# Performance work log

Hardware: AMD Instinct MI355X
Metric: run time of the kernel (lower is better)

The kernel has to match this reference:

```python
import jax, jax.numpy as jnp
import numpy as np

B, N, K, U = 64, 4096, 32, 16
NUM_STEPS = 8
NUM_CLASSES = 2


def setup_inputs() -> dict:
    key = jax.random.key(0)
    ks = jax.random.split(key, 17)
    s = 0.05
    g = lambda k, shape: jax.random.normal(k, shape, dtype=jnp.float32) * s
    return {
        "inputs": jax.random.normal(ks[0], (B, N, K + 2), dtype=jnp.float32),
        # UGRNN cell params
        "Wn": g(ks[1], (K, U)),
        "Wg": g(ks[2], (U, U)), "Ug": g(ks[3], (U, U)), "bg": jnp.zeros((U,), jnp.float32),
        "Wc": g(ks[4], (U, U)), "Uc": g(ks[5], (U, U)), "bc": jnp.zeros((U,), jnp.float32),
        "We": g(ks[6], (U, U)), "be": jnp.zeros((U,), jnp.float32),
        # MLP head (Dropout is identity at inference)
        "W1": g(ks[7], (N * U, 256)), "b1": jnp.zeros((256,), jnp.float32),
        "W2": g(ks[8], (256, 32)),    "b2": jnp.zeros((32,), jnp.float32),
        "W3": g(ks[9], (32, NUM_CLASSES)), "b3": jnp.zeros((NUM_CLASSES,), jnp.float32),
    }


def reference(inputs, Wn, Wg, Ug, bg, Wc, Uc, bc, We, be, W1, b1, W2, b2, W3, b3):
    # split channels: node scalar, K neighbour features, edge scalar
    h0 = inputs[..., 0]            # [B, N]
    neigh = inputs[..., 1:-1]      # [B, N, K]
    e0 = inputs[..., -1]           # [B, N]

    units = Wg.shape[0]
    h = jnp.broadcast_to(h0[..., None], h0.shape + (units,))  # tile -> [B, N, U]
    e = jnp.broadcast_to(e0[..., None], e0.shape + (units,))  # tile -> [B, N, U]

    # neighbour aggregation/projection is constant across steps -> hoist
    m = jnp.einsum("bnk,ku->bnu", neigh, Wn)  # [B, N, U]

    for _ in range(NUM_STEPS):  # small fixed unroll over num_steps
        x = m + e
        g = jax.nn.sigmoid(x @ Wg + h @ Ug + bg)  # update gate
        c = jnp.tanh(x @ Wc + h @ Uc + bc)        # candidate
        h = g * h + (1.0 - g) * c                 # UGRNN update
        e = jnp.tanh(x @ We + be)                 # edge state update

    out = h.reshape(h.shape[0], -1)               # Flatten -> [B, N*U]
    out = jax.nn.relu(out @ W1 + b1)
    out = jax.nn.relu(out @ W2 + b2)
    return jax.nn.softmax(out @ W3 + b3, axis=-1)  # [B, num_classes]
```

## Files before the change

kernel.cpp:

```cpp
#include <hip/hip_runtime.h>

typedef _Float16 half8_t __attribute__((ext_vector_type(8)));
typedef _Float16 half4_t __attribute__((ext_vector_type(4)));
typedef __fp16   fp16x2  __attribute__((ext_vector_type(2)));
typedef float    f32x4  __attribute__((ext_vector_type(4)));

#define MFMA32(a, b, c) __builtin_amdgcn_mfma_f32_16x16x32_f16((a), (b), (c), 0, 0, 0)
#define MFMA16(a, b, c) __builtin_amdgcn_mfma_f32_16x16x16f16((a), (b), (c), 0, 0, 0)

__device__ __forceinline__ void load_lds16(const void* g, void* l) {
    __builtin_amdgcn_global_load_lds(
        (const __attribute__((address_space(1))) unsigned int*)g,
        (__attribute__((address_space(3))) unsigned int*)l, 16, 0, 0);
}
__device__ __forceinline__ void load_lds4(const void* g, void* l) {
    __builtin_amdgcn_global_load_lds(
        (const __attribute__((address_space(1))) unsigned int*)g,
        (__attribute__((address_space(3))) unsigned int*)l, 4, 0, 0);
}

__device__ __forceinline__ half4_t pk4(f32x4 v) {
    fp16x2 lo = __builtin_amdgcn_cvt_pkrtz(v[0], v[1]);
    fp16x2 hi = __builtin_amdgcn_cvt_pkrtz(v[2], v[3]);
    half4_t r;
    r[0] = (_Float16)lo[0]; r[1] = (_Float16)lo[1];
    r[2] = (_Float16)hi[0]; r[3] = (_Float16)hi[1];
    return r;
}

__device__ __forceinline__ f32x4 exp2v(f32x4 v) {
    f32x4 r;
    r[0] = __builtin_amdgcn_exp2f(v[0]);
    r[1] = __builtin_amdgcn_exp2f(v[1]);
    r[2] = __builtin_amdgcn_exp2f(v[2]);
    r[3] = __builtin_amdgcn_exp2f(v[3]);
    return r;
}
__device__ __forceinline__ f32x4 rcpv(f32x4 v) {
    f32x4 r;
    r[0] = __builtin_amdgcn_rcpf(v[0]);
    r[1] = __builtin_amdgcn_rcpf(v[1]);
    r[2] = __builtin_amdgcn_rcpf(v[2]);
    r[3] = __builtin_amdgcn_rcpf(v[3]);
    return r;
}

__global__
__attribute__((amdgpu_flat_work_group_size(256, 256)))
void ugrnn_mfma(
    const float* __restrict__ inputs,
    const float* __restrict__ Wn, const float* __restrict__ Wg,
    const float* __restrict__ Ug, const float* __restrict__ bg,
    const float* __restrict__ Wc, const float* __restrict__ Uc,
    const float* __restrict__ bc, const float* __restrict__ We,
    const float* __restrict__ be, _Float16* __restrict__ h_t)
{
    __shared__ float raw[4][1088];

    const int wave = threadIdx.x >> 6;
    const int lane = threadIdx.x & 63;
    const int t16  = lane & 15;
    const int q    = lane >> 4;

    const int pair = blockIdx.x * 4 + wave;
    const int b    = pair >> 7;
    const int n0   = (pair & 127) << 5;

    const float* gsrc = inputs + (size_t)pair * 1088;
    float* buf = raw[wave];
#pragma unroll
    for (int k2 = 0; k2 < 4; ++k2)
        load_lds16(gsrc + k2 * 256 + lane * 4, buf + k2 * 256);
    load_lds4(gsrc + 1024 + lane, buf + 1024);

    const float NL2E = -1.44269504f;
    const float TL2E =  2.88539008f;

    half8_t An;
#pragma unroll
    for (int i = 0; i < 8; ++i)
        An[i] = (_Float16)Wn[(q * 8 + i) * 16 + t16];

    half4_t Awg, Aug, Awc, Auc, Awe;
#pragma unroll
    for (int i = 0; i < 4; ++i) {
        const int k = 4 * q + i;
        Awg[i] = (_Float16)(Wg[k * 16 + t16] * NL2E);
        Aug[i] = (_Float16)(Ug[k * 16 + t16] * NL2E);
        Awc[i] = (_Float16)(Wc[k * 16 + t16] * TL2E);
        Auc[i] = (_Float16)(Uc[k * 16 + t16] * TL2E);
        Awe[i] = (_Float16)(We[k * 16 + t16] * TL2E);
    }
    f32x4 bgC, bcC, beC;
#pragma unroll
    for (int r = 0; r < 4; ++r) {
        bgC[r] = bg[4 * q + r] * NL2E;
        bcC[r] = bc[4 * q + r] * TL2E;
        beC[r] = be[4 * q + r] * TL2E;
    }

    asm volatile("s_waitcnt vmcnt(0)" ::: "memory");
    __builtin_amdgcn_sched_barrier(0);

    f32x4 m[2], h[2], e[2];
    const f32x4 zc = {0.f, 0.f, 0.f, 0.f};
#pragma unroll
    for (int u2 = 0; u2 < 2; ++u2) {
        const float* rp = buf + u2 * 544;
        half8_t Bx;
#pragma unroll
        for (int i = 0; i < 8; ++i)
            Bx[i] = (_Float16)rp[t16 * 34 + 1 + q * 8 + i];
        m[u2] = MFMA32(An, Bx, zc);
        const float hv = rp[t16 * 34 + 0];
        const float ev = rp[t16 * 34 + 33];
        h[u2] = (f32x4){hv, hv, hv, hv};
        e[u2] = (f32x4){ev, ev, ev, ev};
    }

    const f32x4 one = {1.f, 1.f, 1.f, 1.f};

#pragma unroll 1
    for (int step = 0; step < 8; ++step) {
        f32x4 gp[2], cp[2], ep[2];
#pragma unroll
        for (int u2 = 0; u2 < 2; ++u2) {
            const f32x4 x = m[u2] + e[u2];
            half4_t xB = pk4(x);
            half4_t hB = pk4(h[u2]);
            f32x4 g1 = MFMA16(Awg, xB, bgC);
            f32x4 g2 = MFMA16(Aug, hB, zc);
            f32x4 c1 = MFMA16(Awc, xB, bcC);
            f32x4 c2 = MFMA16(Auc, hB, zc);
            gp[u2] = g1 + g2;
            cp[u2] = c1 + c2;
            if (step < 7) ep[u2] = MFMA16(Awe, xB, beC);
        }
#pragma unroll
        for (int u2 = 0; u2 < 2; ++u2) {
            const f32x4 Ae = one + exp2v(gp[u2]);
            const f32x4 Be = one + exp2v(cp[u2]);
            if (step < 7) {
                const f32x4 Ce = one + exp2v(ep[u2]);
                const f32x4 BC = Be * Ce;
                const f32x4 rr = rcpv(Ae * BC);
                const f32x4 gv = rr * BC;
                const f32x4 cv = one - 2.0f * (rr * (Ae * Ce));
                h[u2] = cv + gv * (h[u2] - cv);
                e[u2] = one - 2.0f * (rr * (Ae * Be));
            } else {
                const f32x4 rr = rcpv(Ae * Be);
                const f32x4 gv = rr * Be;
                const f32x4 cv = one - 2.0f * (rr * Ae);
                h[u2] = cv + gv * (h[u2] - cv);
            }
        }
    }

#pragma unroll
    for (int u2 = 0; u2 < 2; ++u2)
        *(half4_t*)(h_t + (size_t)b * 65536
                        + (size_t)(n0 + u2 * 16 + t16) * 16 + 4 * q) =
            pk4(h[u2]);
}

__global__
__attribute__((amdgpu_flat_work_group_size(256, 256)))
void fc1_mfma(const _Float16* __restrict__ h_t, const float* __restrict__ W1,
              _Float16* __restrict__ partials)
{
    __shared__ float w1s[2][32][258];
    const int tid  = threadIdx.x;
    const int wave = tid >> 6;
    const int lane = tid & 63;
    const int t16  = lane & 15;
    const int q    = lane >> 4;
    const int i0   = blockIdx.x * 128;

    f32x4 acc[4][4];
#pragma unroll
    for (int mt = 0; mt < 4; ++mt)
#pragma unroll
        for (int nt = 0; nt < 4; ++nt)
            acc[mt][nt] = (f32x4){0.f, 0.f, 0.f, 0.f};

#pragma unroll
    for (int r = 0; r < 8; ++r) {
        int row = wave * 8 + r;
        load_lds16(W1 + (size_t)(i0 + row) * 256 + lane * 4, &w1s[0][row][0]);
    }
    __syncthreads();

#pragma unroll 1
    for (int c = 0; c < 4; ++c) {
        const int buf = c & 1;
        const int cb  = i0 + c * 32;

        half8_t A[4];
#pragma unroll
        for (int mt = 0; mt < 4; ++mt)
            A[mt] = *(const half8_t*)(h_t
                + (size_t)(mt * 16 + t16) * 65536 + cb + q * 8);

        if (c < 3) {
#pragma unroll
            for (int r = 0; r < 8; ++r) {
                int row = wave * 8 + r;
                load_lds16(W1 + (size_t)(cb + 32 + row) * 256 + lane * 4,
                           &w1s[buf ^ 1][row][0]);
            }
        }

#pragma unroll
        for (int nt = 0; nt < 4; ++nt) {
            int j = (wave * 4 + nt) * 16 + t16;
            half8_t Bf;
#pragma unroll
            for (int i = 0; i < 8; ++i)
                Bf[i] = (_Float16)w1s[buf][q * 8 + i][j];
#pragma unroll
            for (int mt = 0; mt < 4; ++mt)
                acc[mt][nt] = MFMA32(A[mt], Bf, acc[mt][nt]);
        }
        __syncthreads();
    }

    _Float16* pb = partials + (size_t)blockIdx.x * 16384;
#pragma unroll
    for (int mt = 0; mt < 4; ++mt)
#pragma unroll
        for (int nt = 0; nt < 4; ++nt)
#pragma unroll
            for (int r = 0; r < 4; ++r)
                pb[(mt * 16 + 4 * q + r) * 256 + (wave * 4 + nt) * 16 + t16] =
                    (_Float16)acc[mt][nt][r];
}

__global__ __launch_bounds__(1024) void mlp_tail(
    const _Float16* __restrict__ partials, const float* __restrict__ b1,
    const float* __restrict__ W2, const float* __restrict__ b2,
    const float* __restrict__ W3, const float* __restrict__ b3,
    float* __restrict__ out)
{
    __shared__ float x1p[16][256];
    __shared__ float x1s[256];
    __shared__ float x2q[32][33];
    __shared__ float x2s[32];
    __shared__ float lg[2];
    const int b = blockIdx.x, tid = threadIdx.x;
    const int kg = tid >> 6, l64 = tid & 63;
    const int j0 = l64 * 4;

    const _Float16* p = partials + (size_t)(kg * 32) * 16384 + (size_t)b * 256 + j0;
    float s0 = 0.f, s1 = 0.f, s2 = 0.f, s3 = 0.f;
#pragma unroll
    for (int k = 0; k < 32; ++k) {
        half4_t v = *(const half4_t*)(p + (size_t)k * 16384);
        s0 += (float)v[0]; s1 += (float)v[1]; s2 += (float)v[2]; s3 += (float)v[3];
    }
    x1p[kg][j0 + 0] = s0;
    x1p[kg][j0 + 1] = s1;
    x1p[kg][j0 + 2] = s2;
    x1p[kg][j0 + 3] = s3;
    __syncthreads();

    if (tid < 256) {
        float t = b1[tid];
#pragma unroll
        for (int g = 0; g < 16; ++g) t += x1p[g][tid];
        x1s[tid] = fmaxf(t, 0.f);
    }
    __syncthreads();

    const int j2 = tid & 31, g2 = tid >> 5;
    float s = 0.f;
#pragma unroll
    for (int k = g2 * 8; k < g2 * 8 + 8; ++k) s += x1s[k] * W2[k * 32 + j2];
    x2q[g2][j2] = s;
    __syncthreads();
    if (tid < 32) {
        float t = b2[tid];
#pragma unroll
        for (int g = 0; g < 32; ++g) t += x2q[g][tid];
        x2s[tid] = fmaxf(t, 0.f);
    }
    __syncthreads();
    if (tid < 2) {
        float t = b3[tid];
#pragma unroll
        for (int k = 0; k < 32; ++k) t += x2s[k] * W3[k * 2 + tid];
        lg[tid] = t;
    }
    __syncthreads();
    if (tid == 0) {
        float mx = fmaxf(lg[0], lg[1]);
        float e0 = __expf(lg[0] - mx), e1 = __expf(lg[1] - mx);
        float inv = 1.0f / (e0 + e1);
        out[b * 2 + 0] = e0 * inv;
        out[b * 2 + 1] = e1 * inv;
    }
}

extern "C" void kernel_launch(void* const* d_in, const int* in_sizes, int n_in,
                              void* d_out, int out_size, void* d_ws, size_t ws_size,
                              hipStream_t stream) {
    const float* inputs = (const float*)d_in[0];
    const float* Wn = (const float*)d_in[1];
    const float* Wg = (const float*)d_in[2];
    const float* Ug = (const float*)d_in[3];
    const float* bg = (const float*)d_in[4];
    const float* Wc = (const float*)d_in[5];
    const float* Uc = (const float*)d_in[6];
    const float* bc = (const float*)d_in[7];
    const float* We = (const float*)d_in[8];
    const float* be = (const float*)d_in[9];
    const float* W1 = (const float*)d_in[10];
    const float* b1 = (const float*)d_in[11];
    const float* W2 = (const float*)d_in[12];
    const float* b2 = (const float*)d_in[13];
    const float* W3 = (const float*)d_in[14];
    const float* b3 = (const float*)d_in[15];
    float* out = (float*)d_out;

    _Float16* h_t      = (_Float16*)d_ws;
    _Float16* partials = (_Float16*)((char*)d_ws + (size_t)64 * 65536 * 2);

    ugrnn_mfma<<<2048, 256, 0, stream>>>(inputs, Wn, Wg, Ug, bg, Wc, Uc, bc,
                                         We, be, h_t);
    fc1_mfma<<<512, 256, 0, stream>>>(h_t, W1, partials);
    mlp_tail<<<64, 1024, 0, stream>>>(partials, b1, W2, b2, W3, b3, out);
}
```

Measured before the change: 185.2 us.

## Fuse UGRNN recurrence with FC1 partial GEMM in one kernel

Merges the recurrence kernel and the first dense layer into one kernel. Each block now handles 4 nodes across all 64 batches, keeps h in LDS, and multiplies it directly against the matching 64 rows of W1, so the h_t round trip through global memory and one launch go away. The cost is a partials buffer 1024-deep instead of 512-deep, which makes the tail reduction read twice as many partials. W1 is now read straight from global memory with strided scalar loads instead of being staged through LDS, and the block grows to 512 threads with a waves-per-EU hint.

After: 246.9 us. 1.33x slower.

```diff
diff --git a/kernel.cpp b/kernel.cpp
--- a/kernel.cpp
+++ b/kernel.cpp
@@ -7,17 +7,6 @@
 
 #define MFMA32(a, b, c) __builtin_amdgcn_mfma_f32_16x16x32_f16((a), (b), (c), 0, 0, 0)
 #define MFMA16(a, b, c) __builtin_amdgcn_mfma_f32_16x16x16f16((a), (b), (c), 0, 0, 0)
-
-__device__ __forceinline__ void load_lds16(const void* g, void* l) {
-    __builtin_amdgcn_global_load_lds(
-        (const __attribute__((address_space(1))) unsigned int*)g,
-        (__attribute__((address_space(3))) unsigned int*)l, 16, 0, 0);
-}
-__device__ __forceinline__ void load_lds4(const void* g, void* l) {
-    __builtin_amdgcn_global_load_lds(
-        (const __attribute__((address_space(1))) unsigned int*)g,
-        (__attribute__((address_space(3))) unsigned int*)l, 4, 0, 0);
-}
 
 __device__ __forceinline__ half4_t pk4(f32x4 v) {
     fp16x2 lo = __builtin_amdgcn_cvt_pkrtz(v[0], v[1]);
@@ -27,7 +16,6 @@
     r[2] = (_Float16)hi[0]; r[3] = (_Float16)hi[1];
     return r;
 }
-
 __device__ __forceinline__ f32x4 exp2v(f32x4 v) {
     f32x4 r;
     r[0] = __builtin_amdgcn_exp2f(v[0]);
@@ -46,32 +34,47 @@
 }
 
 __global__
-__attribute__((amdgpu_flat_work_group_size(256, 256)))
-void ugrnn_mfma(
+__attribute__((amdgpu_flat_work_group_size(512, 512), amdgpu_waves_per_eu(6, 8)))
+void ugrnn_fc1(
     const float* __restrict__ inputs,
     const float* __restrict__ Wn, const float* __restrict__ Wg,
     const float* __restrict__ Ug, const float* __restrict__ bg,
     const float* __restrict__ Wc, const float* __restrict__ Uc,
     const float* __restrict__ bc, const float* __restrict__ We,
-    const float* __restrict__ be, _Float16* __restrict__ h_t)
+    const float* __restrict__ be, const float* __restrict__ W1,
+    _Float16* __restrict__ partials)
 {
-    __shared__ float raw[4][1088];
-
-    const int wave = threadIdx.x >> 6;
-    const int lane = threadIdx.x & 63;
+    __shared__ _Float16 neigh[256][40];
+    __shared__ float    he[256][2];
+    __shared__ _Float16 hs[64][72];
+
+    const int tid  = threadIdx.x;
+    const int wave = tid >> 6;
+    const int lane = tid & 63;
     const int t16  = lane & 15;
     const int q    = lane >> 4;
-
-    const int pair = blockIdx.x * 4 + wave;
-    const int b    = pair >> 7;
-    const int n0   = (pair & 127) << 5;
-
-    const float* gsrc = inputs + (size_t)pair * 1088;
-    float* buf = raw[wave];
-#pragma unroll
-    for (int k2 = 0; k2 < 4; ++k2)
-        load_lds16(gsrc + k2 * 256 + lane * 4, buf + k2 * 256);
-    load_lds4(gsrc + 1024 + lane, buf + 1024);
+    const int bk   = blockIdx.x;
+    const int n0   = bk << 2;
+
+    {
+        const int ss = tid >> 1;
+        const int hf = tid & 1;
+        const int sb = ss & 63;
+        const int sn = ss >> 6;
+        const float* row = inputs + ((size_t)sb * 4096 + (n0 + sn)) * 34 + hf * 17;
+        float d[17];
+#pragma unroll
+        for (int i = 0; i < 17; ++i) d[i] = row[i];
+        if (hf == 0) he[ss][0] = d[0];
+        else         he[ss][1] = d[16];
+        const int c0 = hf << 4;
+#pragma unroll
+        for (int j = 0; j < 16; j += 2) {
+            float a = (hf == 0) ? d[1 + j] : d[j];
+            float b = (hf == 0) ? d[2 + j] : d[j + 1];
+            *(fp16x2*)&neigh[ss][c0 + j] = __builtin_amdgcn_cvt_pkrtz(a, b);
+        }
+    }
 
     const float NL2E = -1.44269504f;
     const float TL2E =  2.88539008f;
@@ -99,21 +102,21 @@
         beC[r] = be[4 * q + r] * TL2E;
     }
 
-    asm volatile("s_waitcnt vmcnt(0)" ::: "memory");
-    __builtin_amdgcn_sched_barrier(0);
+    __syncthreads();
+
+    const float* pfp = W1 + (size_t)bk * 16384 + tid * 32;
+    float pf0 = pfp[0], pf1 = pfp[16];
 
     f32x4 m[2], h[2], e[2];
     const f32x4 zc = {0.f, 0.f, 0.f, 0.f};
 #pragma unroll
     for (int u2 = 0; u2 < 2; ++u2) {
-        const float* rp = buf + u2 * 544;
-        half8_t Bx;
-#pragma unroll
-        for (int i = 0; i < 8; ++i)
-            Bx[i] = (_Float16)rp[t16 * 34 + 1 + q * 8 + i];
+        const int T = wave * 2 + u2;
+        const int s = T * 16 + t16;
+        half8_t Bx = *(const half8_t*)&neigh[s][q * 8];
         m[u2] = MFMA32(An, Bx, zc);
-        const float hv = rp[t16 * 34 + 0];
-        const float ev = rp[t16 * 34 + 33];
+        const float hv = he[s][0];
+        const float ev = he[s][1];
         h[u2] = (f32x4){hv, hv, hv, hv};
         e[u2] = (f32x4){ev, ev, ev, ev};
     }
@@ -158,82 +161,52 @@
     }
 
 #pragma unroll
-    for (int u2 = 0; u2 < 2; ++u2)
-        *(half4_t*)(h_t + (size_t)b * 65536
-                        + (size_t)(n0 + u2 * 16 + t16) * 16 + 4 * q) =
-            pk4(h[u2]);
-}
-
-__global__
-__attribute__((amdgpu_flat_work_group_size(256, 256)))
-void fc1_mfma(const _Float16* __restrict__ h_t, const float* __restrict__ W1,
-              _Float16* __restrict__ partials)
-{
-    __shared__ float w1s[2][32][258];
-    const int tid  = threadIdx.x;
-    const int wave = tid >> 6;
-    const int lane = tid & 63;
-    const int t16  = lane & 15;
-    const int q    = lane >> 4;
-    const int i0   = blockIdx.x * 128;
-
-    f32x4 acc[4][4];
+    for (int u2 = 0; u2 < 2; ++u2) {
+        const int T = wave * 2 + u2;
+        *(half4_t*)&hs[(T & 3) * 16 + t16][(T >> 2) * 16 + q * 4] = pk4(h[u2]);
+    }
+    __syncthreads();
+
+    f32x4 acc[4][2];
 #pragma unroll
     for (int mt = 0; mt < 4; ++mt)
 #pragma unroll
-        for (int nt = 0; nt < 4; ++nt)
-            acc[mt][nt] = (f32x4){0.f, 0.f, 0.f, 0.f};
-
-#pragma unroll
-    for (int r = 0; r < 8; ++r) {
-        int row = wave * 8 + r;
-        load_lds16(W1 + (size_t)(i0 + row) * 256 + lane * 4, &w1s[0][row][0]);
-    }
-    __syncthreads();
-
-#pragma unroll 1
-    for (int c = 0; c < 4; ++c) {
-        const int buf = c & 1;
-        const int cb  = i0 + c * 32;
-
+        for (int jt = 0; jt < 2; ++jt)
+            acc[mt][jt] = (f32x4){0.f, 0.f, 0.f, 0.f};
+
+    const int j0w = wave * 32;
+#pragma unroll
+    for (int ks = 0; ks < 2; ++ks) {
         half8_t A[4];
 #pragma unroll
         for (int mt = 0; mt < 4; ++mt)
-            A[mt] = *(const half8_t*)(h_t
-                + (size_t)(mt * 16 + t16) * 65536 + cb + q * 8);
-
-        if (c < 3) {
-#pragma unroll
-            for (int r = 0; r < 8; ++r) {
-                int row = wave * 8 + r;
-                load_lds16(W1 + (size_t)(cb + 32 + row) * 256 + lane * 4,
-                           &w1s[buf ^ 1][row][0]);
-            }
-        }
-
-#pragma unroll
-        for (int nt = 0; nt < 4; ++nt) {
-            int j = (wave * 4 + nt) * 16 + t16;
+            A[mt] = *(const half8_t*)&hs[mt * 16 + t16][ks * 32 + q * 8];
+#pragma unroll
+        for (int jt = 0; jt < 2; ++jt) {
+            const float* wp = W1
+                + (size_t)(bk * 64 + ks * 32 + q * 8) * 256 + j0w + jt * 16 + t16;
             half8_t Bf;
 #pragma unroll
             for (int i = 0; i < 8; ++i)
-                Bf[i] = (_Float16)w1s[buf][q * 8 + i][j];
+                Bf[i] = (_Float16)wp[i * 256];
 #pragma unroll
             for (int mt = 0; mt < 4; ++mt)
-                acc[mt][nt] = MFMA32(A[mt], Bf, acc[mt][nt]);
-        }
-        __syncthreads();
-    }
-
-    _Float16* pb = partials + (size_t)blockIdx.x * 16384;
+                acc[mt][jt] = MFMA32(A[mt], Bf, acc[mt][jt]);
+        }
+    }
+
 #pragma unroll
     for (int mt = 0; mt < 4; ++mt)
 #pragma unroll
-        for (int nt = 0; nt < 4; ++nt)
+        for (int jt = 0; jt < 2; ++jt) {
+            half4_t hv = pk4(acc[mt][jt]);
 #pragma unroll
             for (int r = 0; r < 4; ++r)
-                pb[(mt * 16 + 4 * q + r) * 256 + (wave * 4 + nt) * 16 + t16] =
-                    (_Float16)acc[mt][nt][r];
+                partials[((size_t)(mt * 16 + q * 4 + r) * 1024 + bk) * 256
+                         + j0w + jt * 16 + t16] = hv[r];
+        }
+
+    asm volatile("" :: "v"(pf0), "v"(pf1));
 }
 
 __global__ __launch_bounds__(1024) void mlp_tail(
@@ -251,11 +224,12 @@
     const int kg = tid >> 6, l64 = tid & 63;
     const int j0 = l64 * 4;
 
-    const _Float16* p = partials + (size_t)(kg * 32) * 16384 + (size_t)b * 256 + j0;
+    const _Float16* p = partials + (size_t)b * 262144
+                      + (size_t)(kg * 64) * 256 + j0;
     float s0 = 0.f, s1 = 0.f, s2 = 0.f, s3 = 0.f;
-#pragma unroll
-    for (int k = 0; k < 32; ++k) {
-        half4_t v = *(const half4_t*)(p + (size_t)k * 16384);
+#pragma unroll 8
+    for (int k = 0; k < 64; ++k) {
+        half4_t v = *(const half4_t*)(p + (size_t)k * 256);
         s0 += (float)v[0]; s1 += (float)v[1]; s2 += (float)v[2]; s3 += (float)v[3];
     }
     x1p[kg][j0 + 0] = s0;
@@ -322,11 +296,9 @@
     const float* b3 = (const float*)d_in[15];
     float* out = (float*)d_out;
 
-    _Float16* h_t      = (_Float16*)d_ws;
-    _Float16* partials = (_Float16*)((char*)d_ws + (size_t)64 * 65536 * 2);
-
-    ugrnn_mfma<<<2048, 256, 0, stream>>>(inputs, Wn, Wg, Ug, bg, Wc, Uc, bc,
-                                         We, be, h_t);
-    fc1_mfma<<<512, 256, 0, stream>>>(h_t, W1, partials);
+    _Float16* partials = (_Float16*)d_ws;
+
+    ugrnn_fc1<<<1024, 512, 0, stream>>>(inputs, Wn, Wg, Ug, bg, Wc, Uc, bc,
+                                        We, be, W1, partials);
     mlp_tail<<<64, 1024, 0, stream>>>(partials, b1, W2, b2, W3, b3, out);
 }
```
